# Optimization experiments

Measured on AMD Instinct MI355X. Metric: run time of the kernel, lower is better.

The kernel has to match this reference:

```python
import jax, jax.numpy as jnp
import numpy as np
from jax import lax

B, C, H, W = 32, 64, 112, 112
ALPHA, BETA1, BETA2 = 0.25, 1.0, 1.0

# STE sign for weights (DifferntiableSign): fwd = +/-1, bwd mask |w|<=1 (w in [-1,1))
@jax.custom_vjp
def dsign(w):
    return jnp.where(w >= 0, 1.0, -1.0).astype(w.dtype)
def _dsign_fwd(w):
    return dsign(w), w
def _dsign_bwd(w, g):
    return (g * ((w < 1) & (w >= -1)).astype(g.dtype),)
dsign.defvjp(_dsign_fwd, _dsign_bwd)

# ReActNet BinaryActivation: fwd = sign(x), bwd piecewise-polynomial STE
@jax.custom_vjp
def bin_act(x):
    return jnp.where(x >= 0, 1.0, -1.0).astype(x.dtype)
def _ba_fwd(x):
    return bin_act(x), x
def _ba_bwd(x, g):
    slope = jnp.where((x >= -1) & (x < 0), 2.0 + 2.0 * x,
             jnp.where((x >= 0) & (x < 1), 2.0 - 2.0 * x, 0.0))
    return (g * slope.astype(g.dtype),)
bin_act.defvjp(_ba_fwd, _ba_bwd)

def scaled_sign_conv(x, w):
    # per-output-channel scale = mean(|w|) over (in, kh, kw)
    scale = jnp.mean(jnp.abs(w), axis=(1, 2, 3), keepdims=True)
    wb = scale * dsign(w)
    return lax.conv_general_dilated(x, wb, window_strides=(1, 1),
                                    padding=((1, 1), (1, 1)),
                                    dimension_numbers=("NCHW", "OIHW", "NCHW"))

def add_bias(x, b):
    return x + b[None, :, None, None]

def prelu(x, a):
    return jnp.where(x >= 0, x, a[None, :, None, None] * x)

def setup_inputs() -> dict:
    key = jax.random.key(0)
    ks = jax.random.split(key, 12)
    x = jax.random.normal(ks[0], (B, C, H, W), dtype=jnp.float32)
    # conv weights: symmetric uniform in [-1e-3, 1e-3] so signs are nontrivial
    w3 = (jax.random.uniform(ks[1], (C, C, 3, 3)) - 0.5) * 0.002
    w_pw = (jax.random.uniform(ks[2], (C, C, 3, 3)) - 0.5) * 0.002
    b11 = jax.random.normal(ks[3], (C,)) * 0.01
    b12 = jax.random.normal(ks[4], (C,)) * 0.01
    b13 = jax.random.normal(ks[5], (C,)) * 0.01
    b21 = jax.random.normal(ks[6], (C,)) * 0.01
    b22 = jax.random.normal(ks[7], (C,)) * 0.01
    b23 = jax.random.normal(ks[8], (C,)) * 0.01
    a1 = jax.random.uniform(ks[9], (C,), minval=0.1, maxval=0.4)
    a2 = jax.random.uniform(ks[10], (C,), minval=0.1, maxval=0.4)
    return {"x": x, "w3": w3, "w_pw": w_pw, "b11": b11, "b12": b12, "b13": b13,
            "b21": b21, "b22": b22, "b23": b23, "a1": a1, "a2": a2}

def reference(x, w3, w_pw, b11, b12, b13, b21, b22, b23, a1, a2):
    x_in = x * BETA1
    out1 = add_bias(x_in, b11)            # move11
    out1 = bin_act(out1)
    out1 = scaled_sign_conv(out1, w3)     # binary_3x3
    out1 = x + out1 * ALPHA               # stride==1: residual is original x
    out1 = add_bias(out1, b12)            # move12
    out1 = prelu(out1, a1)
    out1 = add_bias(out1, b13)            # move13
    out1_in = out1 * BETA2
    out2 = add_bias(out1_in, b21)         # move21
    out2 = bin_act(out2)
    out2 = scaled_sign_conv(out2, w_pw)   # binary_pw (3x3 per given defaults)
    out2 = out2 * ALPHA + out1
    out2 = add_bias(out2, b22)            # move22
    out2 = prelu(out2, a2)
    out2 = add_bias(out2, b23)            # move23
    return out2
```

## Files before the change

kernel.cpp:

```cpp
#include <hip/hip_runtime.h>
#include <stdint.h>

#define Bn 32
#define Cc 64
#define Hh 112
#define Ww 112
#define HWp (Hh*Ww)
#define NPIX (Bn*HWp)
#define ALPHA 0.25f

#define WB1_OFF   0
#define WB2_OFF   4608
#define SC1_OFF   9216
#define SC2_OFF   9472
#define BITS1_OFF 16384
#define BITS2_OFF (16384 + 3211264)

__global__ void prep_weights(const float* __restrict__ w, uint64_t* __restrict__ wbits,
                             float* __restrict__ scale) {
    int o = threadIdx.x;
    uint64_t m[9] = {0,0,0,0,0,0,0,0,0};
    float asum = 0.f;
    const float* wo = w + o * Cc * 9;
    for (int i = 0; i < Cc; ++i) {
        #pragma unroll
        for (int t = 0; t < 9; ++t) {
            float v = wo[i * 9 + t];
            asum += fabsf(v);
            if (v < 0.f) m[t] |= (1ull << i);
        }
    }
    #pragma unroll
    for (int t = 0; t < 9; ++t) wbits[o * 9 + t] = m[t];
    scale[o] = asum * (1.f / 576.f);
}

__global__ void pack1(const float* __restrict__ x, const float* __restrict__ b11,
                      uint64_t* __restrict__ bits) {
    int idx = blockIdx.x * 256 + threadIdx.x;
    int n = idx / HWp, hw = idx % HWp;
    const float* xp = x + (size_t)n * Cc * HWp + hw;
    uint64_t m = 0;
    #pragma unroll 8
    for (int c = 0; c < Cc; ++c) {
        float v = xp[(size_t)c * HWp] + b11[c];
        if (v < 0.f) m |= (1ull << c);
    }
    bits[idx] = m;
}

__device__ __forceinline__ void load_neigh(const uint64_t* __restrict__ bp,
                                           int h, int w, uint64_t xm[9], int vm[9],
                                           int& nvalid) {
    nvalid = 0;
    #pragma unroll
    for (int t = 0; t < 9; ++t) {
        int dh = t / 3 - 1, dw = t % 3 - 1;
        int hh = h + dh, ww = w + dw;
        bool ok = (hh >= 0) & (hh < Hh) & (ww >= 0) & (ww < Ww);
        xm[t] = ok ? bp[hh * Ww + ww] : 0ull;
        vm[t] = ok ? -1 : 0;
        nvalid += ok ? 1 : 0;
    }
}

__global__ void conv1_ep(const float* __restrict__ x,
                         const uint64_t* __restrict__ bits1,
                         const uint64_t* __restrict__ wb,
                         const float* __restrict__ sc,
                         const float* __restrict__ b12, const float* __restrict__ a1,
                         const float* __restrict__ b13, const float* __restrict__ b21,
                         float* __restrict__ out1, uint64_t* __restrict__ bits2) {
    int idx = blockIdx.x * 256 + threadIdx.x;
    int n = idx / HWp, hw = idx % HWp;
    int h = hw / Ww, w = hw % Ww;
    uint64_t xm[9]; int vm[9]; int nvalid;
    load_neigh(bits1 + (size_t)n * HWp, h, w, xm, vm, nvalid);

    const float* xp = x + (size_t)n * Cc * HWp + hw;
    float* op = out1 + (size_t)n * Cc * HWp + hw;
    uint64_t m2 = 0;
    for (int o = 0; o < Cc; ++o) {
        int s = 0;
        #pragma unroll
        for (int t = 0; t < 9; ++t)
            s += __builtin_popcountll(xm[t] ^ wb[o * 9 + t]) & vm[t];
        int dot = (nvalid << 6) - (s << 1);
        float conv = sc[o] * (float)dot;
        float v = xp[(size_t)o * HWp] + ALPHA * conv;
        v += b12[o];
        v = v >= 0.f ? v : a1[o] * v;
        v += b13[o];
        op[(size_t)o * HWp] = v;
        if (v + b21[o] < 0.f) m2 |= (1ull << o);
    }
    bits2[idx] = m2;
}

__global__ void conv2_ep(const uint64_t* __restrict__ bits2,
                         const uint64_t* __restrict__ wb,
                         const float* __restrict__ sc,
                         const float* __restrict__ b22, const float* __restrict__ a2,
                         const float* __restrict__ b23,
                         float* __restrict__ io) {
    int idx = blockIdx.x * 256 + threadIdx.x;
    int n = idx / HWp, hw = idx % HWp;
    int h = hw / Ww, w = hw % Ww;
    uint64_t xm[9]; int vm[9]; int nvalid;
    load_neigh(bits2 + (size_t)n * HWp, h, w, xm, vm, nvalid);

    float* iop = io + (size_t)n * Cc * HWp + hw;
    for (int o = 0; o < Cc; ++o) {
        int s = 0;
        #pragma unroll
        for (int t = 0; t < 9; ++t)
            s += __builtin_popcountll(xm[t] ^ wb[o * 9 + t]) & vm[t];
        int dot = (nvalid << 6) - (s << 1);
        float conv = sc[o] * (float)dot;
        float v = ALPHA * conv + iop[(size_t)o * HWp];
        v += b22[o];
        v = v >= 0.f ? v : a2[o] * v;
        v += b23[o];
        iop[(size_t)o * HWp] = v;
    }
}

extern "C" void kernel_launch(void* const* d_in, const int* in_sizes, int n_in,
                              void* d_out, int out_size, void* d_ws, size_t ws_size,
                              hipStream_t stream) {
    const float* x    = (const float*)d_in[0];
    const float* w3   = (const float*)d_in[1];
    const float* wpw  = (const float*)d_in[2];
    const float* b11  = (const float*)d_in[3];
    const float* b12  = (const float*)d_in[4];
    const float* b13  = (const float*)d_in[5];
    const float* b21  = (const float*)d_in[6];
    const float* b22  = (const float*)d_in[7];
    const float* b23  = (const float*)d_in[8];
    const float* a1   = (const float*)d_in[9];
    const float* a2   = (const float*)d_in[10];

    char* ws = (char*)d_ws;
    uint64_t* wb1   = (uint64_t*)(ws + WB1_OFF);
    uint64_t* wb2   = (uint64_t*)(ws + WB2_OFF);
    float*    sc1   = (float*)(ws + SC1_OFF);
    float*    sc2   = (float*)(ws + SC2_OFF);
    uint64_t* bits1 = (uint64_t*)(ws + BITS1_OFF);
    uint64_t* bits2 = (uint64_t*)(ws + BITS2_OFF);
    float*    out   = (float*)d_out;

    const int nblk = NPIX / 256;

    prep_weights<<<1, 64, 0, stream>>>(w3,  wb1, sc1);
    prep_weights<<<1, 64, 0, stream>>>(wpw, wb2, sc2);
    pack1<<<nblk, 256, 0, stream>>>(x, b11, bits1);
    conv1_ep<<<nblk, 256, 0, stream>>>(x, bits1, wb1, sc1, b12, a1, b13, b21, out, bits2);
    conv2_ep<<<nblk, 256, 0, stream>>>(bits2, wb2, sc2, b22, a2, b23, out);
}
```

Baseline: 339.5 us.

## Process four pixels per thread with sliding bit windows and float4 access

Each thread now handles four adjacent pixels, loading a shared 3x6 window of packed bit masks so neighbor loads are reused across outputs, and the per-o weight words are reused across four pixels. Activation reads and writes use float4 and packed mask stores use 128-bit writes. Weight prep is parallelized into 128 blocks using wave ballots and shuffles, merged into one launch. This cuts redundant neighbor loads and instruction overhead, at the cost of higher register pressure and fewer threads.

```diff
diff --git a/kernel.cpp b/kernel.cpp
--- a/kernel.cpp
+++ b/kernel.cpp
@@ -7,6 +7,9 @@
 #define Ww 112
 #define HWp (Hh*Ww)
 #define NPIX (Bn*HWp)
+#define GPR (Ww/4)
+#define GPI (GPR*Hh)
+#define NGRP (Bn*GPI)
 #define ALPHA 0.25f
 
 #define WB1_OFF   0
@@ -16,112 +19,188 @@
 #define BITS1_OFF 16384
 #define BITS2_OFF (16384 + 3211264)
 
-__global__ void prep_weights(const float* __restrict__ w, uint64_t* __restrict__ wbits,
-                             float* __restrict__ scale) {
-    int o = threadIdx.x;
-    uint64_t m[9] = {0,0,0,0,0,0,0,0,0};
+__global__ __launch_bounds__(64) void prep_weights(
+        const float* __restrict__ w3, const float* __restrict__ wpw,
+        uint64_t* __restrict__ wb1, uint64_t* __restrict__ wb2,
+        float* __restrict__ sc1, float* __restrict__ sc2) {
+    int b = blockIdx.x;
+    int lane = threadIdx.x;
+    const float* w   = (b < 64) ? w3  : wpw;
+    uint64_t* wbits  = (b < 64) ? wb1 : wb2;
+    float*    scale  = (b < 64) ? sc1 : sc2;
+    int o = b & 63;
+    const float* wp = w + ((size_t)o * Cc + lane) * 9;
+    float v[9];
     float asum = 0.f;
-    const float* wo = w + o * Cc * 9;
-    for (int i = 0; i < Cc; ++i) {
-        #pragma unroll
-        for (int t = 0; t < 9; ++t) {
-            float v = wo[i * 9 + t];
-            asum += fabsf(v);
-            if (v < 0.f) m[t] |= (1ull << i);
-        }
-    }
-    #pragma unroll
-    for (int t = 0; t < 9; ++t) wbits[o * 9 + t] = m[t];
-    scale[o] = asum * (1.f / 576.f);
-}
-
-__global__ void pack1(const float* __restrict__ x, const float* __restrict__ b11,
-                      uint64_t* __restrict__ bits) {
-    int idx = blockIdx.x * 256 + threadIdx.x;
-    int n = idx / HWp, hw = idx % HWp;
-    const float* xp = x + (size_t)n * Cc * HWp + hw;
-    uint64_t m = 0;
+    #pragma unroll
+    for (int t = 0; t < 9; ++t) { v[t] = wp[t]; asum += fabsf(v[t]); }
+    uint64_t mym = 0;
+    #pragma unroll
+    for (int t = 0; t < 9; ++t) {
+        uint64_t bal = __ballot(v[t] < 0.f);
+        if (lane == t) mym = bal;
+    }
+    if (lane < 9) wbits[o * 9 + lane] = mym;
+    #pragma unroll
+    for (int off = 32; off > 0; off >>= 1) asum += __shfl_down(asum, off, 64);
+    if (lane == 0) scale[o] = asum * (1.f / 576.f);
+}
+
+__global__ __launch_bounds__(128) void pack1(const float* __restrict__ x,
+                                             const float* __restrict__ b11,
+                                             uint64_t* __restrict__ bits) {
+    int gid = blockIdx.x * 128 + threadIdx.x;
+    int n = gid / (HWp / 4);
+    int r = gid - n * (HWp / 4);
+    size_t base = (size_t)n * Cc * HWp + (size_t)r * 4;
+    uint64_t m0 = 0, m1 = 0, m2 = 0, m3 = 0;
     #pragma unroll 8
     for (int c = 0; c < Cc; ++c) {
-        float v = xp[(size_t)c * HWp] + b11[c];
-        if (v < 0.f) m |= (1ull << c);
-    }
-    bits[idx] = m;
-}
-
-__device__ __forceinline__ void load_neigh(const uint64_t* __restrict__ bp,
-                                           int h, int w, uint64_t xm[9], int vm[9],
-                                           int& nvalid) {
-    nvalid = 0;
-    #pragma unroll
-    for (int t = 0; t < 9; ++t) {
-        int dh = t / 3 - 1, dw = t % 3 - 1;
-        int hh = h + dh, ww = w + dw;
-        bool ok = (hh >= 0) & (hh < Hh) & (ww >= 0) & (ww < Ww);
-        xm[t] = ok ? bp[hh * Ww + ww] : 0ull;
-        vm[t] = ok ? -1 : 0;
-        nvalid += ok ? 1 : 0;
-    }
-}
-
-__global__ void conv1_ep(const float* __restrict__ x,
-                         const uint64_t* __restrict__ bits1,
-                         const uint64_t* __restrict__ wb,
-                         const float* __restrict__ sc,
-                         const float* __restrict__ b12, const float* __restrict__ a1,
-                         const float* __restrict__ b13, const float* __restrict__ b21,
-                         float* __restrict__ out1, uint64_t* __restrict__ bits2) {
-    int idx = blockIdx.x * 256 + threadIdx.x;
-    int n = idx / HWp, hw = idx % HWp;
-    int h = hw / Ww, w = hw % Ww;
-    uint64_t xm[9]; int vm[9]; int nvalid;
-    load_neigh(bits1 + (size_t)n * HWp, h, w, xm, vm, nvalid);
-
-    const float* xp = x + (size_t)n * Cc * HWp + hw;
-    float* op = out1 + (size_t)n * Cc * HWp + hw;
-    uint64_t m2 = 0;
+        float4 v = *(const float4*)(x + base + (size_t)c * HWp);
+        float bc = b11[c];
+        uint64_t bit = 1ull << c;
+        if (v.x + bc < 0.f) m0 |= bit;
+        if (v.y + bc < 0.f) m1 |= bit;
+        if (v.z + bc < 0.f) m2 |= bit;
+        if (v.w + bc < 0.f) m3 |= bit;
+    }
+    uint64_t* bp = bits + (size_t)n * HWp + (size_t)r * 4;
+    ulonglong2* bp2 = (ulonglong2*)bp;
+    bp2[0] = make_ulonglong2(m0, m1);
+    bp2[1] = make_ulonglong2(m2, m3);
+}
+
+__device__ __forceinline__ void load_window(const uint64_t* __restrict__ bp,
+                                            int h, int w0,
+                                            uint64_t win[3][6], int vmx[3][6],
+                                            int nvalid[4]) {
+    int vc0 = (w0 > 0) ? -1 : 0;
+    int vc5 = (w0 < Ww - 4) ? -1 : 0;
+    #pragma unroll
+    for (int dh = 0; dh < 3; ++dh) {
+        int hh = h + dh - 1;
+        bool okr = (hh >= 0) & (hh < Hh);
+        int vr = okr ? -1 : 0;
+        const uint64_t* rp = bp + hh * Ww + (w0 - 1);
+        #pragma unroll
+        for (int c = 0; c < 6; ++c) {
+            int vcc = (c == 0) ? vc0 : (c == 5) ? vc5 : -1;
+            int m = vr & vcc;
+            vmx[dh][c] = m;
+            win[dh][c] = (m != 0) ? rp[c] : 0ull;
+        }
+    }
+    #pragma unroll
+    for (int p = 0; p < 4; ++p) {
+        int nv = 0;
+        #pragma unroll
+        for (int dh = 0; dh < 3; ++dh)
+            #pragma unroll
+            for (int dw = 0; dw < 3; ++dw)
+                nv += vmx[dh][p + dw] & 1;
+        nvalid[p] = nv;
+    }
+}
+
+__global__ __launch_bounds__(128) void conv1_ep(
+        const float* __restrict__ x, const uint64_t* __restrict__ bits1,
+        const uint64_t* __restrict__ wb, const float* __restrict__ sc,
+        const float* __restrict__ b12, const float* __restrict__ a1,
+        const float* __restrict__ b13, const float* __restrict__ b21,
+        float* __restrict__ out1, uint64_t* __restrict__ bits2) {
+    int gid = blockIdx.x * 128 + threadIdx.x;
+    int n = gid / GPI;
+    int r = gid - n * GPI;
+    int h = r / GPR;
+    int w0 = (r - h * GPR) * 4;
+
+    uint64_t win[3][6]; int vmx[3][6]; int nvalid[4];
+    load_window(bits1 + (size_t)n * HWp, h, w0, win, vmx, nvalid);
+
+    size_t pbase = (size_t)n * Cc * HWp + h * Ww + w0;
+    const float* xp = x + pbase;
+    float* op = out1 + pbase;
+    uint64_t m2[4] = {0, 0, 0, 0};
+
     for (int o = 0; o < Cc; ++o) {
-        int s = 0;
-        #pragma unroll
-        for (int t = 0; t < 9; ++t)
-            s += __builtin_popcountll(xm[t] ^ wb[o * 9 + t]) & vm[t];
-        int dot = (nvalid << 6) - (s << 1);
-        float conv = sc[o] * (float)dot;
-        float v = xp[(size_t)o * HWp] + ALPHA * conv;
-        v += b12[o];
-        v = v >= 0.f ? v : a1[o] * v;
-        v += b13[o];
-        op[(size_t)o * HWp] = v;
-        if (v + b21[o] < 0.f) m2 |= (1ull << o);
-    }
-    bits2[idx] = m2;
-}
-
-__global__ void conv2_ep(const uint64_t* __restrict__ bits2,
-                         const uint64_t* __restrict__ wb,
-                         const float* __restrict__ sc,
-                         const float* __restrict__ b22, const float* __restrict__ a2,
-                         const float* __restrict__ b23,
-                         float* __restrict__ io) {
-    int idx = blockIdx.x * 256 + threadIdx.x;
-    int n = idx / HWp, hw = idx % HWp;
-    int h = hw / Ww, w = hw % Ww;
-    uint64_t xm[9]; int vm[9]; int nvalid;
-    load_neigh(bits2 + (size_t)n * HWp, h, w, xm, vm, nvalid);
-
-    float* iop = io + (size_t)n * Cc * HWp + hw;
+        const uint64_t* wbo = wb + o * 9;
+        int s0 = 0, s1 = 0, s2 = 0, s3 = 0;
+        #pragma unroll
+        for (int dh = 0; dh < 3; ++dh) {
+            #pragma unroll
+            for (int dw = 0; dw < 3; ++dw) {
+                uint64_t wv = wbo[dh * 3 + dw];
+                s0 += __popcll(win[dh][0 + dw] ^ wv) & vmx[dh][0 + dw];
+                s1 += __popcll(win[dh][1 + dw] ^ wv) & vmx[dh][1 + dw];
+                s2 += __popcll(win[dh][2 + dw] ^ wv) & vmx[dh][2 + dw];
+                s3 += __popcll(win[dh][3 + dw] ^ wv) & vmx[dh][3 + dw];
+            }
+        }
+        float asc = ALPHA * sc[o];
+        float4 xv = *(const float4*)(xp + (size_t)o * HWp);
+        float v0 = xv.x + asc * (float)((nvalid[0] << 6) - 2 * s0);
+        float v1 = xv.y + asc * (float)((nvalid[1] << 6) - 2 * s1);
+        float v2 = xv.z + asc * (float)((nvalid[2] << 6) - 2 * s2);
+        float v3 = xv.w + asc * (float)((nvalid[3] << 6) - 2 * s3);
+        float bb = b12[o], aa = a1[o], cc = b13[o], d21 = b21[o];
+        v0 += bb; v0 = v0 >= 0.f ? v0 : aa * v0; v0 += cc;
+        v1 += bb; v1 = v1 >= 0.f ? v1 : aa * v1; v1 += cc;
+        v2 += bb; v2 = v2 >= 0.f ? v2 : aa * v2; v2 += cc;
+        v3 += bb; v3 = v3 >= 0.f ? v3 : aa * v3; v3 += cc;
+        *(float4*)(op + (size_t)o * HWp) = make_float4(v0, v1, v2, v3);
+        uint64_t bit = 1ull << o;
+        if (v0 + d21 < 0.f) m2[0] |= bit;
+        if (v1 + d21 < 0.f) m2[1] |= bit;
+        if (v2 + d21 < 0.f) m2[2] |= bit;
+        if (v3 + d21 < 0.f) m2[3] |= bit;
+    }
+    ulonglong2* bq = (ulonglong2*)(bits2 + (size_t)n * HWp + h * Ww + w0);
+    bq[0] = make_ulonglong2(m2[0], m2[1]);
+    bq[1] = make_ulonglong2(m2[2], m2[3]);
+}
+
+__global__ __launch_bounds__(128) void conv2_ep(
+        const uint64_t* __restrict__ bits2,
+        const uint64_t* __restrict__ wb, const float* __restrict__ sc,
+        const float* __restrict__ b22, const float* __restrict__ a2,
+        const float* __restrict__ b23, float* __restrict__ io) {
+    int gid = blockIdx.x * 128 + threadIdx.x;
+    int n = gid / GPI;
+    int r = gid - n * GPI;
+    int h = r / GPR;
+    int w0 = (r - h * GPR) * 4;
+
+    uint64_t win[3][6]; int vmx[3][6]; int nvalid[4];
+    load_window(bits2 + (size_t)n * HWp, h, w0, win, vmx, nvalid);
+
+    float* iop = io + (size_t)n * Cc * HWp + h * Ww + w0;
+
     for (int o = 0; o < Cc; ++o) {
-        int s = 0;
-        #pragma unroll
-        for (int t = 0; t < 9; ++t)
-            s += __builtin_popcountll(xm[t] ^ wb[o * 9 + t]) & vm[t];
-        int dot = (nvalid << 6) - (s << 1);
-        float conv = sc[o] * (float)dot;
-        float v = ALPHA * conv + iop[(size_t)o * HWp];
-        v += b22[o];
-        v = v >= 0.f ? v : a2[o] * v;
-        v += b23[o];
-        iop[(size_t)o * HWp] = v;
+        const uint64_t* wbo = wb + o * 9;
+        int s0 = 0, s1 = 0, s2 = 0, s3 = 0;
+        #pragma unroll
+        for (int dh = 0; dh < 3; ++dh) {
+            #pragma unroll
+            for (int dw = 0; dw < 3; ++dw) {
+                uint64_t wv = wbo[dh * 3 + dw];
+                s0 += __popcll(win[dh][0 + dw] ^ wv) & vmx[dh][0 + dw];
+                s1 += __popcll(win[dh][1 + dw] ^ wv) & vmx[dh][1 + dw];
+                s2 += __popcll(win[dh][2 + dw] ^ wv) & vmx[dh][2 + dw];
+                s3 += __popcll(win[dh][3 + dw] ^ wv) & vmx[dh][3 + dw];
+            }
+        }
+        float asc = ALPHA * sc[o];
+        float4 rv = *(const float4*)(iop + (size_t)o * HWp);
+        float v0 = rv.x + asc * (float)((nvalid[0] << 6) - 2 * s0);
+        float v1 = rv.y + asc * (float)((nvalid[1] << 6) - 2 * s1);
+        float v2 = rv.z + asc * (float)((nvalid[2] << 6) - 2 * s2);
+        float v3 = rv.w + asc * (float)((nvalid[3] << 6) - 2 * s3);
+        float bb = b22[o], aa = a2[o], cc = b23[o];
+        v0 += bb; v0 = v0 >= 0.f ? v0 : aa * v0; v0 += cc;
+        v1 += bb; v1 = v1 >= 0.f ? v1 : aa * v1; v1 += cc;
+        v2 += bb; v2 = v2 >= 0.f ? v2 : aa * v2; v2 += cc;
+        v3 += bb; v3 = v3 >= 0.f ? v3 : aa * v3; v3 += cc;
+        *(float4*)(iop + (size_t)o * HWp) = make_float4(v0, v1, v2, v3);
     }
 }
 
@@ -149,11 +228,8 @@
     uint64_t* bits2 = (uint64_t*)(ws + BITS2_OFF);
     float*    out   = (float*)d_out;
 
-    const int nblk = NPIX / 256;
-
-    prep_weights<<<1, 64, 0, stream>>>(w3,  wb1, sc1);
-    prep_weights<<<1, 64, 0, stream>>>(wpw, wb2, sc2);
-    pack1<<<nblk, 256, 0, stream>>>(x, b11, bits1);
-    conv1_ep<<<nblk, 256, 0, stream>>>(x, bits1, wb1, sc1, b12, a1, b13, b21, out, bits2);
-    conv2_ep<<<nblk, 256, 0, stream>>>(bits2, wb2, sc2, b22, a2, b23, out);
-}
+    prep_weights<<<128, 64, 0, stream>>>(w3, wpw, wb1, wb2, sc1, sc2);
+    pack1<<<NGRP / 128, 128, 0, stream>>>(x, b11, bits1);
+    conv1_ep<<<NGRP / 128, 128, 0, stream>>>(x, bits1, wb1, sc1, b12, a1, b13, b21, out, bits2);
+    conv2_ep<<<NGRP / 128, 128, 0, stream>>>(bits2, wb2, sc2, b22, a2, b23, out);
+}
```

Result: faster. 328.7 us (-3.2%).
